# Performance work log

Measured on AMD Instinct MI355X. Metric: run time of the kernel, lower is better.

The kernel has to match this reference:

```python
import jax, jax.numpy as jnp
import numpy as np

BETA = 0.1  # sliced_fgw_distance default (forward does not override it)
EPS = 1e-12  # F.normalize eps


def setup_inputs() -> dict:
    key = jax.random.key(0)
    k1, k2, k3 = jax.random.split(key, 3)
    N, D, P = 2048, 512, 10
    z = jax.random.normal(k1, (N, D), dtype=jnp.float32)
    gmm_noise = jax.random.normal(k2, (N, D), dtype=jnp.float32)
    projections = jax.random.normal(k3, (D, P), dtype=jnp.float32)
    return {"z": z, "gmm_noise": gmm_noise, "projections": projections}


def _pairwise_sq_diff(a):
    # a: [N, P] -> [N, N, P] of (a_i - a_j)^2  (p=2, so abs()**2 == square)
    return (a[:, None, :] - a[None, :, :]) ** 2


def reference(z, gmm_noise, projections):
    # gmm_samples = F.normalize(randn_like(z)) : L2-normalize rows
    norm = jnp.maximum(jnp.linalg.norm(gmm_noise, axis=1, keepdims=True), EPS)
    gmm_samples = gmm_noise / norm  # [N, D]

    post = jnp.sort(z @ projections, axis=0)            # [N, P] ascending
    prior_proj = gmm_samples @ projections              # [N, P]
    prior1 = jnp.sort(prior_proj, axis=0)               # ascending
    prior2 = prior1[::-1]                               # descending sort

    post_diff = _pairwise_sq_diff(post)                 # [N, N, P]
    gw1 = jnp.mean((post_diff - _pairwise_sq_diff(prior1)) ** 2, axis=(0, 1))  # [P]
    gw2 = jnp.mean((post_diff - _pairwise_sq_diff(prior2)) ** 2, axis=(0, 1))  # [P]

    w1 = jnp.sum((post - prior1) ** 2, axis=0)          # [P]
    w2 = jnp.sum((post - prior2) ** 2, axis=0)          # [P]

    fgw1 = (1.0 - BETA) * w1 + BETA * gw1
    fgw2 = (1.0 - BETA) * w2 + BETA * gw2
    return jnp.mean(jnp.minimum(fgw1, fgw2))
```

## Files before the change

### kernel.cpp

```cpp
#include <hip/hip_runtime.h>
#include <math.h>

#define N_ROWS 2048
#define D_DIM 512
#define P_DIM 10

__device__ inline float wave_reduce_f(float v) {
#pragma unroll
  for (int off = 32; off > 0; off >>= 1) v += __shfl_down(v, off, 64);
  return v;
}

__device__ inline double wave_reduce_d(double v) {
#pragma unroll
  for (int off = 32; off > 0; off >>= 1) v += __shfl_down(v, off, 64);
  return v;
}

__global__ __launch_bounds__(256) void rc_proj_kernel(
    const float* __restrict__ z, const float* __restrict__ g,
    const float* __restrict__ proj, float* __restrict__ post_cm,
    float* __restrict__ prior_cm) {
  __shared__ float pl[P_DIM * D_DIM];
  for (int i = threadIdx.x; i < P_DIM * D_DIM; i += 256) {
    int k = i / P_DIM, p = i - k * P_DIM;
    pl[p * D_DIM + k] = proj[i];
  }
  __syncthreads();
  const int wave = threadIdx.x >> 6, lane = threadIdx.x & 63;
  const int row = blockIdx.x * 4 + wave;
  const float* zr = z + (size_t)row * D_DIM;
  const float* gr = g + (size_t)row * D_DIM;
  float zv[8], gv[8];
#pragma unroll
  for (int m = 0; m < 8; ++m) {
    zv[m] = zr[m * 64 + lane];
    gv[m] = gr[m * 64 + lane];
  }
  float n2 = 0.f;
#pragma unroll
  for (int m = 0; m < 8; ++m) n2 += gv[m] * gv[m];
  float az[P_DIM], ag[P_DIM];
#pragma unroll
  for (int p = 0; p < P_DIM; ++p) { az[p] = 0.f; ag[p] = 0.f; }
#pragma unroll
  for (int m = 0; m < 8; ++m) {
#pragma unroll
    for (int p = 0; p < P_DIM; ++p) {
      float w = pl[p * D_DIM + m * 64 + lane];
      az[p] += zv[m] * w;
      ag[p] += gv[m] * w;
    }
  }
#pragma unroll
  for (int p = 0; p < P_DIM; ++p) {
    az[p] = wave_reduce_f(az[p]);
    ag[p] = wave_reduce_f(ag[p]);
  }
  n2 = wave_reduce_f(n2);
  if (lane == 0) {
    float inv = 1.f / fmaxf(sqrtf(n2), 1e-12f);
    for (int p = 0; p < P_DIM; ++p) {
      post_cm[p * N_ROWS + row] = az[p];
      prior_cm[p * N_ROWS + row] = ag[p] * inv;
    }
  }
}

__global__ __launch_bounds__(1024) void rc_sort_kernel(
    float* __restrict__ post_cm, float* __restrict__ prior_cm) {
  float* buf = (blockIdx.x < P_DIM) ? post_cm + blockIdx.x * N_ROWS
                                    : prior_cm + (blockIdx.x - P_DIM) * N_ROWS;
  __shared__ float s[N_ROWS];
  const int tid = threadIdx.x;
  s[tid] = buf[tid];
  s[tid + 1024] = buf[tid + 1024];
  for (unsigned k = 2; k <= N_ROWS; k <<= 1) {
    for (unsigned j = k >> 1; j > 0; j >>= 1) {
      __syncthreads();
#pragma unroll
      for (int t = 0; t < 2; ++t) {
        unsigned idx = (unsigned)tid + (unsigned)t * 1024u;
        unsigned ixj = idx ^ j;
        if (ixj > idx) {
          float x = s[idx], y = s[ixj];
          bool up = (idx & k) == 0;
          if (up ? (x > y) : (x < y)) { s[idx] = y; s[ixj] = x; }
        }
      }
    }
  }
  __syncthreads();
  buf[tid] = s[tid];
  buf[tid + 1024] = s[tid + 1024];
}

__global__ __launch_bounds__(256) void rc_stats_kernel(
    const float* __restrict__ post_cm, const float* __restrict__ prior_cm,
    float* __restrict__ fgw) {
  const int p = blockIdx.x % P_DIM;
  const int variant = blockIdx.x / P_DIM;
  const float* a = post_cm + p * N_ROWS;
  const float* b = prior_cm + p * N_ROWS;
  double S[10];
#pragma unroll
  for (int t = 0; t < 10; ++t) S[t] = 0.0;
  for (int i = threadIdx.x; i < N_ROWS; i += 256) {
    double av = (double)a[i];
    double bv = (double)(variant ? b[N_ROWS - 1 - i] : b[i]);
    double a2 = av * av, b2 = bv * bv;
    double s = a2 - b2;
    S[0] += s * s;
    S[1] += s;
    S[2] += s * av;
    S[3] += av;
    S[4] += s * bv;
    S[5] += bv;
    S[6] += a2;
    S[7] += av * bv;
    S[8] += b2;
    double d = av - bv;
    S[9] += d * d;
  }
#pragma unroll
  for (int t = 0; t < 10; ++t) S[t] = wave_reduce_d(S[t]);
  __shared__ double sm[4][10];
  const int wave = threadIdx.x >> 6, lane = threadIdx.x & 63;
  if (lane == 0) {
#pragma unroll
    for (int t = 0; t < 10; ++t) sm[wave][t] = S[t];
  }
  __syncthreads();
  if (threadIdx.x == 0) {
    double T[10];
#pragma unroll
    for (int t = 0; t < 10; ++t)
      T[t] = sm[0][t] + sm[1][t] + sm[2][t] + sm[3][t];
    const double nn = (double)N_ROWS;
    double gw = (2.0 * nn * T[0] + 2.0 * T[1] * T[1]
                 - 8.0 * (T[2] * T[3] - T[4] * T[5])
                 + 4.0 * (T[6] * T[6] - 2.0 * T[7] * T[7] + T[8] * T[8]))
                / (nn * nn);
    double w = T[9];
    fgw[blockIdx.x] = (float)(0.9 * w + 0.1 * gw);
  }
}

__global__ void rc_final_kernel(const float* __restrict__ fgw,
                                float* __restrict__ out) {
  if (threadIdx.x == 0 && blockIdx.x == 0) {
    float s = 0.f;
    for (int p = 0; p < P_DIM; ++p) s += fminf(fgw[p], fgw[P_DIM + p]);
    out[0] = s * (1.f / P_DIM);
  }
}

extern "C" void kernel_launch(void* const* d_in, const int* in_sizes, int n_in,
                              void* d_out, int out_size, void* d_ws,
                              size_t ws_size, hipStream_t stream) {
  const float* z = (const float*)d_in[0];
  const float* g = (const float*)d_in[1];
  const float* proj = (const float*)d_in[2];
  float* out = (float*)d_out;
  float* post_cm = (float*)d_ws;
  float* prior_cm = post_cm + N_ROWS * P_DIM;
  float* fgw = prior_cm + N_ROWS * P_DIM;

  rc_proj_kernel<<<N_ROWS / 4, 256, 0, stream>>>(z, g, proj, post_cm, prior_cm);
  rc_sort_kernel<<<2 * P_DIM, 1024, 0, stream>>>(post_cm, prior_cm);
  rc_stats_kernel<<<2 * P_DIM, 256, 0, stream>>>(post_cm, prior_cm, fgw);
  rc_final_kernel<<<1, 64, 0, stream>>>(fgw, out);
}
```

Measured before the change: 92.87 us.

## Fuse sort, stats and final reduction into one kernel; vectorize projection loads

Merges the sort, stats and final kernels into one kernel per projection. Each block sorts both the post and prior columns in shared memory, then computes power-sum moments from which both the ascending and reversed-prior FGW values are derived, and atomically adds the minimum into the output. The bitonic sort now gives each thread one compare-exchange per stage and uses a wave-level fence instead of a block barrier for strides below 64. The projection kernel loads rows as float4 and zeroes the output. This removes two launches and the global round trip of sorted data, but uses fewer blocks (10 instead of 20) and relies on float atomics and on wave-synchronous shared-memory ordering.

```diff
diff --git a/kernel.cpp b/kernel.cpp
--- a/kernel.cpp
+++ b/kernel.cpp
@@ -17,39 +17,50 @@
   return v;
 }
 
+__device__ inline void wave_lds_fence() {
+  asm volatile("" ::: "memory");
+  __builtin_amdgcn_wave_barrier();
+  asm volatile("" ::: "memory");
+}
+
 __global__ __launch_bounds__(256) void rc_proj_kernel(
-    const float* __restrict__ z, const float* __restrict__ g,
+    const float4* __restrict__ z4, const float4* __restrict__ g4,
     const float* __restrict__ proj, float* __restrict__ post_cm,
-    float* __restrict__ prior_cm) {
+    float* __restrict__ prior_cm, float* __restrict__ out) {
   __shared__ float pl[P_DIM * D_DIM];
   for (int i = threadIdx.x; i < P_DIM * D_DIM; i += 256) {
-    int k = i / P_DIM, p = i - k * P_DIM;
-    pl[p * D_DIM + k] = proj[i];
+    int e = i / P_DIM, p = i - e * P_DIM;
+    pl[p * D_DIM + (e & 3) * 128 + (e >> 2)] = proj[i];
   }
+  if (blockIdx.x == 0 && threadIdx.x == 0) out[0] = 0.f;
   __syncthreads();
   const int wave = threadIdx.x >> 6, lane = threadIdx.x & 63;
   const int row = blockIdx.x * 4 + wave;
-  const float* zr = z + (size_t)row * D_DIM;
-  const float* gr = g + (size_t)row * D_DIM;
-  float zv[8], gv[8];
-#pragma unroll
-  for (int m = 0; m < 8; ++m) {
-    zv[m] = zr[m * 64 + lane];
-    gv[m] = gr[m * 64 + lane];
-  }
-  float n2 = 0.f;
-#pragma unroll
-  for (int m = 0; m < 8; ++m) n2 += gv[m] * gv[m];
+  const float4* zr = z4 + (size_t)row * (D_DIM / 4);
+  const float4* gr = g4 + (size_t)row * (D_DIM / 4);
+  float4 zv[2], gv[2];
+  zv[0] = zr[lane];
+  zv[1] = zr[64 + lane];
+  gv[0] = gr[lane];
+  gv[1] = gr[64 + lane];
+  float n2 = gv[0].x * gv[0].x + gv[0].y * gv[0].y + gv[0].z * gv[0].z +
+             gv[0].w * gv[0].w + gv[1].x * gv[1].x + gv[1].y * gv[1].y +
+             gv[1].z * gv[1].z + gv[1].w * gv[1].w;
   float az[P_DIM], ag[P_DIM];
 #pragma unroll
   for (int p = 0; p < P_DIM; ++p) { az[p] = 0.f; ag[p] = 0.f; }
 #pragma unroll
-  for (int m = 0; m < 8; ++m) {
+  for (int m = 0; m < 2; ++m) {
+    const float zc[4] = {zv[m].x, zv[m].y, zv[m].z, zv[m].w};
+    const float gc[4] = {gv[m].x, gv[m].y, gv[m].z, gv[m].w};
 #pragma unroll
-    for (int p = 0; p < P_DIM; ++p) {
-      float w = pl[p * D_DIM + m * 64 + lane];
-      az[p] += zv[m] * w;
-      ag[p] += gv[m] * w;
+    for (int c = 0; c < 4; ++c) {
+#pragma unroll
+      for (int p = 0; p < P_DIM; ++p) {
+        float w = pl[p * D_DIM + c * 128 + m * 64 + lane];
+        az[p] += zc[c] * w;
+        ag[p] += gc[c] * w;
+      }
     }
   }
 #pragma unroll
@@ -60,6 +71,7 @@
   n2 = wave_reduce_f(n2);
   if (lane == 0) {
     float inv = 1.f / fmaxf(sqrtf(n2), 1e-12f);
+#pragma unroll
     for (int p = 0; p < P_DIM; ++p) {
       post_cm[p * N_ROWS + row] = az[p];
       prior_cm[p * N_ROWS + row] = ag[p] * inv;
@@ -67,107 +79,114 @@
   }
 }
 
-__global__ __launch_bounds__(1024) void rc_sort_kernel(
-    float* __restrict__ post_cm, float* __restrict__ prior_cm) {
-  float* buf = (blockIdx.x < P_DIM) ? post_cm + blockIdx.x * N_ROWS
-                                    : prior_cm + (blockIdx.x - P_DIM) * N_ROWS;
-  __shared__ float s[N_ROWS];
+__device__ inline double fgw_eval(double Sa, double Sb, double Sa2, double Sb2,
+                                  double Sa3, double Sb3, double Sa4,
+                                  double Sb4, double U1, double U2, double U3,
+                                  double U4) {
+  const double n = (double)N_ROWS;
+  double T0 = Sa4 - 2.0 * U4 + Sb4;
+  double T1 = Sa2 - Sb2;
+  double T2 = Sa3 - U3;
+  double T4 = U2 - Sb3;
+  double gw = (2.0 * n * T0 + 2.0 * T1 * T1 - 8.0 * (T2 * Sa - T4 * Sb) +
+               4.0 * (Sa2 * Sa2 - 2.0 * U1 * U1 + Sb2 * Sb2)) /
+              (n * n);
+  double w = Sa2 + Sb2 - 2.0 * U1;
+  return 0.9 * w + 0.1 * gw;
+}
+
+__global__ __launch_bounds__(1024) void rc_sortstats_kernel(
+    const float* __restrict__ post_cm, const float* __restrict__ prior_cm,
+    float* __restrict__ out) {
+  __shared__ float sa[N_ROWS];
+  __shared__ float sb[N_ROWS];
+  __shared__ double sm[16][16];
+  const int p = blockIdx.x;
   const int tid = threadIdx.x;
-  s[tid] = buf[tid];
-  s[tid + 1024] = buf[tid + 1024];
+  sa[tid] = post_cm[p * N_ROWS + tid];
+  sa[tid + 1024] = post_cm[p * N_ROWS + tid + 1024];
+  sb[tid] = prior_cm[p * N_ROWS + tid];
+  sb[tid + 1024] = prior_cm[p * N_ROWS + tid + 1024];
+  __syncthreads();
+  bool prev_big = false;
   for (unsigned k = 2; k <= N_ROWS; k <<= 1) {
     for (unsigned j = k >> 1; j > 0; j >>= 1) {
-      __syncthreads();
-#pragma unroll
-      for (int t = 0; t < 2; ++t) {
-        unsigned idx = (unsigned)tid + (unsigned)t * 1024u;
-        unsigned ixj = idx ^ j;
-        if (ixj > idx) {
-          float x = s[idx], y = s[ixj];
-          bool up = (idx & k) == 0;
-          if (up ? (x > y) : (x < y)) { s[idx] = y; s[ixj] = x; }
-        }
-      }
+      const bool big = (j >= 64);
+      if (big || prev_big)
+        __syncthreads();
+      else
+        wave_lds_fence();
+      unsigned idx = ((tid & ~(j - 1)) << 1) | (tid & (j - 1));
+      unsigned ixj = idx | j;
+      const bool up = (idx & k) == 0;
+      float x = sa[idx], y = sa[ixj];
+      if (up ? (x > y) : (x < y)) { sa[idx] = y; sa[ixj] = x; }
+      float u = sb[idx], v = sb[ixj];
+      if (up ? (u > v) : (u < v)) { sb[idx] = v; sb[ixj] = u; }
+      prev_big = big;
     }
   }
   __syncthreads();
-  buf[tid] = s[tid];
-  buf[tid + 1024] = s[tid + 1024];
-}
-
-__global__ __launch_bounds__(256) void rc_stats_kernel(
-    const float* __restrict__ post_cm, const float* __restrict__ prior_cm,
-    float* __restrict__ fgw) {
-  const int p = blockIdx.x % P_DIM;
-  const int variant = blockIdx.x / P_DIM;
-  const float* a = post_cm + p * N_ROWS;
-  const float* b = prior_cm + p * N_ROWS;
-  double S[10];
+  double S[16];
 #pragma unroll
-  for (int t = 0; t < 10; ++t) S[t] = 0.0;
-  for (int i = threadIdx.x; i < N_ROWS; i += 256) {
-    double av = (double)a[i];
-    double bv = (double)(variant ? b[N_ROWS - 1 - i] : b[i]);
-    double a2 = av * av, b2 = bv * bv;
-    double s = a2 - b2;
-    S[0] += s * s;
-    S[1] += s;
-    S[2] += s * av;
-    S[3] += av;
-    S[4] += s * bv;
-    S[5] += bv;
-    S[6] += a2;
-    S[7] += av * bv;
-    S[8] += b2;
-    double d = av - bv;
-    S[9] += d * d;
+  for (int t = 0; t < 16; ++t) S[t] = 0.0;
+  for (int i = tid; i < N_ROWS; i += 1024) {
+    double a = (double)sa[i];
+    double b = (double)sb[i];
+    double br = (double)sb[N_ROWS - 1 - i];
+    double a2 = a * a, b2 = b * b, br2 = br * br;
+    S[0] += a;
+    S[1] += b;
+    S[2] += a2;
+    S[3] += b2;
+    S[4] += a2 * a;
+    S[5] += b2 * b;
+    S[6] += a2 * a2;
+    S[7] += b2 * b2;
+    S[8] += a * b;
+    S[9] += a2 * b;
+    S[10] += a * b2;
+    S[11] += a2 * b2;
+    S[12] += a * br;
+    S[13] += a2 * br;
+    S[14] += a * br2;
+    S[15] += a2 * br2;
   }
 #pragma unroll
-  for (int t = 0; t < 10; ++t) S[t] = wave_reduce_d(S[t]);
-  __shared__ double sm[4][10];
-  const int wave = threadIdx.x >> 6, lane = threadIdx.x & 63;
+  for (int t = 0; t < 16; ++t) S[t] = wave_reduce_d(S[t]);
+  const int wave = tid >> 6, lane = tid & 63;
   if (lane == 0) {
 #pragma unroll
-    for (int t = 0; t < 10; ++t) sm[wave][t] = S[t];
+    for (int t = 0; t < 16; ++t) sm[wave][t] = S[t];
   }
   __syncthreads();
-  if (threadIdx.x == 0) {
-    double T[10];
+  if (tid == 0) {
+    double T[16];
 #pragma unroll
-    for (int t = 0; t < 10; ++t)
-      T[t] = sm[0][t] + sm[1][t] + sm[2][t] + sm[3][t];
-    const double nn = (double)N_ROWS;
-    double gw = (2.0 * nn * T[0] + 2.0 * T[1] * T[1]
-                 - 8.0 * (T[2] * T[3] - T[4] * T[5])
-                 + 4.0 * (T[6] * T[6] - 2.0 * T[7] * T[7] + T[8] * T[8]))
-                / (nn * nn);
-    double w = T[9];
-    fgw[blockIdx.x] = (float)(0.9 * w + 0.1 * gw);
-  }
-}
-
-__global__ void rc_final_kernel(const float* __restrict__ fgw,
-                                float* __restrict__ out) {
-  if (threadIdx.x == 0 && blockIdx.x == 0) {
-    float s = 0.f;
-    for (int p = 0; p < P_DIM; ++p) s += fminf(fgw[p], fgw[P_DIM + p]);
-    out[0] = s * (1.f / P_DIM);
+    for (int t = 0; t < 16; ++t) {
+      double acc = 0.0;
+      for (int w = 0; w < 16; ++w) acc += sm[w][t];
+      T[t] = acc;
+    }
+    double f1 = fgw_eval(T[0], T[1], T[2], T[3], T[4], T[5], T[6], T[7], T[8],
+                         T[9], T[10], T[11]);
+    double f2 = fgw_eval(T[0], T[1], T[2], T[3], T[4], T[5], T[6], T[7], T[12],
+                         T[13], T[14], T[15]);
+    atomicAdd(out, (float)(fmin(f1, f2) * (1.0 / P_DIM)));
   }
 }
 
 extern "C" void kernel_launch(void* const* d_in, const int* in_sizes, int n_in,
                               void* d_out, int out_size, void* d_ws,
                               size_t ws_size, hipStream_t stream) {
-  const float* z = (const float*)d_in[0];
-  const float* g = (const float*)d_in[1];
+  const float4* z4 = (const float4*)d_in[0];
+  const float4* g4 = (const float4*)d_in[1];
   const float* proj = (const float*)d_in[2];
   float* out = (float*)d_out;
   float* post_cm = (float*)d_ws;
   float* prior_cm = post_cm + N_ROWS * P_DIM;
-  float* fgw = prior_cm + N_ROWS * P_DIM;
 
-  rc_proj_kernel<<<N_ROWS / 4, 256, 0, stream>>>(z, g, proj, post_cm, prior_cm);
-  rc_sort_kernel<<<2 * P_DIM, 1024, 0, stream>>>(post_cm, prior_cm);
-  rc_stats_kernel<<<2 * P_DIM, 256, 0, stream>>>(post_cm, prior_cm, fgw);
-  rc_final_kernel<<<1, 64, 0, stream>>>(fgw, out);
+  rc_proj_kernel<<<N_ROWS / 4, 256, 0, stream>>>(z4, g4, proj, post_cm,
+                                                 prior_cm, out);
+  rc_sortstats_kernel<<<P_DIM, 1024, 0, stream>>>(post_cm, prior_cm, out);
 }
```

Measured after the change: 102.7 us. 1.11x slower.
